# Performance work log

Measured on AMD Instinct MI355X. Metric: run time of the kernel, lower is better.

Reference implementation:

```python
import jax, jax.numpy as jnp
import numpy as np

N_TOKEN = 8192
N_EMBED = 512
DECAY = 0.99
EPS = 1e-08


def setup_inputs() -> dict:
    key = jax.random.key(0)
    k1, k2, k3, k4 = jax.random.split(key, 4)
    inputs = jax.random.normal(k1, (4, 4096, N_EMBED), dtype=jnp.float32)
    key_w = jax.random.normal(k2, (N_TOKEN, N_EMBED), dtype=jnp.float32)
    value_w = jax.random.normal(k3, (N_TOKEN, N_EMBED), dtype=jnp.float32)
    ema_n = jnp.ones((N_TOKEN,), dtype=jnp.float32)
    ema_w = jax.random.normal(k4, (N_TOKEN, N_EMBED), dtype=jnp.float32)
    return {"inputs": inputs, "key_w": key_w, "value_w": value_w,
            "ema_n": ema_n, "ema_w": ema_w}


def reference(inputs, key_w, value_w, ema_n, ema_w):
    size = inputs.shape
    x = inputs.reshape(-1, N_EMBED)  # [T, D]

    # squared euclidean distances to key codebook: [T, n_token]
    dists = (jnp.sum(x * x, axis=-1, keepdims=True)
             + jnp.sum(key_w * key_w, axis=-1)[None, :]
             - 2.0 * jnp.matmul(x, key_w.T))
    indices = jnp.argmin(dists, axis=-1)  # [T] int

    quantized = (x + value_w[indices]).reshape(size)

    # --- training-mode EMA codebook update (torch .data ops, no grad) ---
    T = x.shape[0]
    ratio = float(N_TOKEN) / T
    # cnts[k] = ratio * (#tokens assigned to k)
    cnts = jnp.zeros((N_TOKEN,), dtype=x.dtype).at[indices].add(ratio)
    # ws = one_hot(indices).T @ x scaled by ratio  (segment sum over codes)
    ws = jax.ops.segment_sum(x, indices, num_segments=N_TOKEN) * ratio
    ema_n_new = ema_n * DECAY + (1.0 - DECAY) * cnts
    ema_w_new = ema_w * DECAY + (1.0 - DECAY) * ws
    # renormalize keys (Laplace-smoothed counts)
    n = jnp.sum(ema_n_new)
    sz = (ema_n_new + EPS) / (n + EPS * N_TOKEN) * n
    key_w_new = ema_w_new / sz[:, None]

    return quantized, ema_n_new, ema_w_new, key_w_new
```

## Files before the change

kernel.cpp:

```cpp
#include <hip/hip_runtime.h>

#define N_TOKEN 8192
#define N_EMBED 512
#define T_TOKENS 16384
#define KP 1536
#define MARGIN 0.6f

typedef __bf16 bf16x8 __attribute__((ext_vector_type(8)));
typedef __bf16 bf16x4 __attribute__((ext_vector_type(4)));
typedef float f32x4 __attribute__((ext_vector_type(4)));

__device__ __forceinline__ unsigned int fkey(float f) {
  unsigned int u = __float_as_uint(f);
  return (u & 0x80000000u) ? ~u : (u | 0x80000000u);
}
__device__ __forceinline__ void gl2lds16(const void* gsrc, void* lds) {
  __builtin_amdgcn_global_load_lds(
      (const __attribute__((address_space(1))) unsigned int*)gsrc,
      (__attribute__((address_space(3))) unsigned int*)lds, 16, 0, 0);
}
__device__ __forceinline__ unsigned long long umin64(unsigned long long a,
                                                     unsigned long long b) {
  return a < b ? a : b;
}

__global__ void k_pack_x(const float* __restrict__ x, __bf16* __restrict__ xp) {
  int gid = blockIdx.x * blockDim.x + threadIdx.x;
  int t = gid >> 7, d4 = gid & 127;
  float4 v = reinterpret_cast<const float4*>(x)[gid];
  bf16x4 hi, lo;
  hi[0] = (__bf16)v.x; hi[1] = (__bf16)v.y; hi[2] = (__bf16)v.z; hi[3] = (__bf16)v.w;
  lo[0] = (__bf16)(v.x - (float)hi[0]);
  lo[1] = (__bf16)(v.y - (float)hi[1]);
  lo[2] = (__bf16)(v.z - (float)hi[2]);
  lo[3] = (__bf16)(v.w - (float)hi[3]);
  __bf16* row = xp + (size_t)t * KP + d4 * 4;
  *(bf16x4*)(row)        = hi;
  *(bf16x4*)(row + 512)  = hi;
  *(bf16x4*)(row + 1024) = lo;
}

__global__ void k_pack_k_norm(const float* __restrict__ kw, __bf16* __restrict__ kp,
                              float* __restrict__ h) {
  int row = blockIdx.x * 4 + (threadIdx.x >> 6);
  int lane = threadIdx.x & 63;
  const float4* src = reinterpret_cast<const float4*>(kw + (size_t)row * N_EMBED);
  __bf16* dst = kp + (size_t)row * KP;
  float s = 0.f;
  #pragma unroll
  for (int c = 0; c < 2; ++c) {
    int f4 = lane + c * 64;
    float4 v = src[f4];
    s += v.x*v.x + v.y*v.y + v.z*v.z + v.w*v.w;
    bf16x4 hi, lo;
    hi[0] = (__bf16)v.x; hi[1] = (__bf16)v.y; hi[2] = (__bf16)v.z; hi[3] = (__bf16)v.w;
    lo[0] = (__bf16)(v.x - (float)hi[0]);
    lo[1] = (__bf16)(v.y - (float)hi[1]);
    lo[2] = (__bf16)(v.z - (float)hi[2]);
    lo[3] = (__bf16)(v.w - (float)hi[3]);
    *(bf16x4*)(dst + f4 * 4)        = hi;
    *(bf16x4*)(dst + 512 + f4 * 4)  = lo;
    *(bf16x4*)(dst + 1024 + f4 * 4) = hi;
  }
  #pragma unroll
  for (int off = 32; off; off >>= 1) s += __shfl_down(s, off);
  if (lane == 0) h[row] = 0.5f * s;
}

__global__ void k_hnorm(const float* __restrict__ key_w, float* __restrict__ h) {
  int code = blockIdx.x * 4 + (threadIdx.x >> 6);
  int lane = threadIdx.x & 63;
  const float4* row = reinterpret_cast<const float4*>(key_w + (size_t)code * N_EMBED);
  float s = 0.f;
  float4 v0 = row[lane];
  float4 v1 = row[lane + 64];
  s += v0.x*v0.x + v0.y*v0.y + v0.z*v0.z + v0.w*v0.w;
  s += v1.x*v1.x + v1.y*v1.y + v1.z*v1.z + v1.w*v1.w;
  #pragma unroll
  for (int off = 32; off; off >>= 1) s += __shfl_down(s, off);
  if (lane == 0) h[code] = 0.5f * s;
}

#define BMr 128
#define BNr 128
#define BKe 64

__global__ __launch_bounds__(256) void k_mfma_top2(
    const __bf16* __restrict__ xp, const __bf16* __restrict__ kp,
    const float* __restrict__ h, float4* __restrict__ slots) {
  __shared__ __bf16 AS[BMr * BKe];
  __shared__ __bf16 BS[BNr * BKe];

  const int nb = blockIdx.x, mb = blockIdx.y;
  const int m0 = mb * BMr, n0 = nb * BNr;
  const int tid = threadIdx.x;
  const int lane = tid & 63;
  const int wid = tid >> 6;
  const int wm = wid * 32;

  f32x4 acc[2][8] = {};
  const int soff = tid * 16;

  for (int ks = 0; ks < 512; ks += BKe) {
    __syncthreads();
    #pragma unroll
    for (int i = 0; i < 4; ++i) {
      int off = i * 4096 + soff;
      int row = off >> 7;
      int inner = (off & 127) ^ ((row & 7) << 4);
      gl2lds16(xp + (size_t)(m0 + row) * KP + ks + (inner >> 1), (char*)AS + off);
      gl2lds16(kp + (size_t)(n0 + row) * KP + ks + (inner >> 1), (char*)BS + off);
    }
    asm volatile("s_waitcnt vmcnt(0)" ::: "memory");
    __syncthreads();

    #pragma unroll
    for (int kk = 0; kk < 2; ++kk) {
      const int cbyte = kk * 64 + (lane >> 4) * 16;
      bf16x8 af[2], bb[8];
      #pragma unroll
      for (int i = 0; i < 2; ++i) {
        int arow = wm + i * 16 + (lane & 15);
        af[i] = *(const bf16x8*)((const char*)AS + arow * 128 + (cbyte ^ ((arow & 7) << 4)));
      }
      #pragma unroll
      for (int j = 0; j < 8; ++j) {
        int brow = j * 16 + (lane & 15);
        bb[j] = *(const bf16x8*)((const char*)BS + brow * 128 + (cbyte ^ ((brow & 7) << 4)));
      }
      #pragma unroll
      for (int i = 0; i < 2; ++i)
        #pragma unroll
        for (int j = 0; j < 8; ++j)
          acc[i][j] = __builtin_amdgcn_mfma_f32_16x16x32_bf16(af[i], bb[j], acc[i][j], 0, 0, 0);
    }
  }

  const int rgrp = lane >> 4;
  const int cidx = lane & 15;
  #pragma unroll
  for (int i = 0; i < 2; ++i) {
    #pragma unroll
    for (int r = 0; r < 4; ++r) {
      float s1 = 3.4e38f, s2 = 3.4e38f;
      int c1 = 0;
      #pragma unroll
      for (int j = 0; j < 8; ++j) {
        int kk = n0 + j * 16 + cidx;
        float sc = h[kk] - acc[i][j][r];
        if (sc < s1) { s2 = s1; s1 = sc; c1 = kk; }
        else s2 = fminf(s2, sc);
      }
      #pragma unroll
      for (int msk = 1; msk < 16; msk <<= 1) {
        float o1 = __shfl_xor(s1, msk);
        float o2 = __shfl_xor(s2, msk);
        int   oc = __shfl_xor(c1, msk);
        float ns2 = fminf(fminf(s2, o2), fmaxf(s1, o1));
        bool take = o1 < s1;
        s1 = take ? o1 : s1;
        c1 = take ? oc : c1;
        s2 = ns2;
      }
      if (cidx == 0) {
        int row = m0 + wm + i * 16 + rgrp * 4 + r;
        float4 p;
        p.x = s1; p.y = s2; p.z = __int_as_float(c1); p.w = 0.f;
        slots[(size_t)row * 64 + nb] = p;
      }
    }
  }
}

__global__ void k_top2_reduce(const float4* __restrict__ slots,
                              int* __restrict__ idx, unsigned int* __restrict__ tlist,
                              unsigned int* __restrict__ ucount,
                              int* __restrict__ counts) {
  int row = blockIdx.x * 4 + (threadIdx.x >> 6);
  int lane = threadIdx.x & 63;
  float4 a = slots[(size_t)row * 64 + lane];
  float s1 = a.x, s2 = a.y; int c1 = __float_as_int(a.z);
  #pragma unroll
  for (int msk = 1; msk < 64; msk <<= 1) {
    float o1 = __shfl_xor(s1, msk);
    float o2 = __shfl_xor(s2, msk);
    int   oc = __shfl_xor(c1, msk);
    float ns2 = fminf(fminf(s2, o2), fmaxf(s1, o1));
    bool take = o1 < s1;
    s1 = take ? o1 : s1;
    c1 = take ? oc : c1;
    s2 = ns2;
  }
  if (lane == 0) {
    if (s2 - s1 >= MARGIN) {
      idx[row] = c1;
      atomicAdd(&counts[c1], 1);
    } else {
      unsigned int p = atomicAdd(ucount, 1u);
      tlist[p] = (unsigned int)row;
    }
  }
}

__global__ __launch_bounds__(256) void k_mfma_refine(
    const __bf16* __restrict__ xp, const __bf16* __restrict__ kp,
    const float* __restrict__ h, const unsigned int* __restrict__ tlist,
    const unsigned int* __restrict__ ucount, unsigned long long* __restrict__ rbest) {
  const unsigned int uc = *ucount;
  const int nb = blockIdx.x, mb = blockIdx.y;
  const int m0 = mb * BMr;
  if ((unsigned int)m0 >= uc) return;

  __shared__ __bf16 AS[BMr * BKe];
  __shared__ __bf16 BS[BNr * BKe];

  const int n0 = nb * BNr;
  const int tid = threadIdx.x;
  const int lane = tid & 63;
  const int wid = tid >> 6;
  const int wm = (wid >> 1) * 64, wn = (wid & 1) * 64;

  const int r0 = tid >> 3;
  size_t abase[4];
  #pragma unroll
  for (int i = 0; i < 4; ++i) {
    int p = m0 + r0 + 32 * i;
    int pc = p < (int)uc ? p : (int)uc - 1;
    abase[i] = (size_t)tlist[pc] * KP;
  }

  f32x4 acc[4][4] = {};
  const int soff = tid * 16;
  const int innerC = (soff & 127) ^ ((r0 & 7) << 4);

  for (int ks = 0; ks < KP; ks += BKe) {
    __syncthreads();
    #pragma unroll
    for (int i = 0; i < 4; ++i) {
      int off = i * 4096 + soff;
      int brow = (off >> 7);
      gl2lds16(xp + abase[i] + ks + (innerC >> 1), (char*)AS + off);
      int binner = (off & 127) ^ ((brow & 7) << 4);
      gl2lds16(kp + (size_t)(n0 + brow) * KP + ks + (binner >> 1), (char*)BS + off);
    }
    asm volatile("s_waitcnt vmcnt(0)" ::: "memory");
    __syncthreads();

    #pragma unroll
    for (int kk = 0; kk < 2; ++kk) {
      const int cbyte = kk * 64 + (lane >> 4) * 16;
      bf16x8 af[4], bb[4];
      #pragma unroll
      for (int i = 0; i < 4; ++i) {
        int arow = wm + i * 16 + (lane & 15);
        af[i] = *(const bf16x8*)((const char*)AS + arow * 128 + (cbyte ^ ((arow & 7) << 4)));
        int brow = wn + i * 16 + (lane & 15);
        bb[i] = *(const bf16x8*)((const char*)BS + brow * 128 + (cbyte ^ ((brow & 7) << 4)));
      }
      #pragma unroll
      for (int i = 0; i < 4; ++i)
        #pragma unroll
        for (int j = 0; j < 4; ++j)
          acc[i][j] = __builtin_amdgcn_mfma_f32_16x16x32_bf16(af[i], bb[j], acc[i][j], 0, 0, 0);
    }
  }

  const int rgrp = lane >> 4;
  const int cidx = lane & 15;
  #pragma unroll
  for (int i = 0; i < 4; ++i) {
    #pragma unroll
    for (int r = 0; r < 4; ++r) {
      unsigned long long m = ~0ull;
      #pragma unroll
      for (int j = 0; j < 4; ++j) {
        int kk = n0 + wn + j * 16 + cidx;
        float score = h[kk] - acc[i][j][r];
        unsigned long long cand =
            ((unsigned long long)fkey(score) << 32) | (unsigned int)kk;
        m = umin64(m, cand);
      }
      #pragma unroll
      for (int msk = 1; msk < 16; msk <<= 1) m = umin64(m, __shfl_xor(m, msk));
      if (cidx == 0) {
        int p = m0 + wm + i * 16 + rgrp * 4 + r;
        if ((unsigned int)p < uc) atomicMin(&rbest[p], m);
      }
    }
  }
}

__global__ void k_finalize(const unsigned long long* __restrict__ rbest,
                           const unsigned int* __restrict__ tlist,
                           const unsigned int* __restrict__ ucount,
                           int* __restrict__ idx, int* __restrict__ counts) {
  unsigned int p = blockIdx.x * 256 + threadIdx.x;
  if (p < *ucount) {
    int k = (int)(unsigned int)(rbest[p] & 0xffffffffull);
    idx[tlist[p]] = k;
    atomicAdd(&counts[k], 1);
  }
}

__global__ void k_sum_ema_n(const float* __restrict__ ema_n, float* __restrict__ nsum) {
  __shared__ float sm[256];
  float s = 0.f;
  for (int i = threadIdx.x; i < N_TOKEN; i += 256) s += ema_n[i];
  sm[threadIdx.x] = s;
  __syncthreads();
  for (int off = 128; off; off >>= 1) {
    if (threadIdx.x < off) sm[threadIdx.x] += sm[threadIdx.x + off];
    __syncthreads();
  }
  if (threadIdx.x == 0) *nsum = sm[0];
}

__global__ void k_scan(const int* __restrict__ counts, int* __restrict__ offs,
                       int* __restrict__ cursor) {
  __shared__ int sa[256], sb[256];
  int tid = threadIdx.x;
  int base = tid * 32;
  int loc[32]; int s = 0;
  #pragma unroll
  for (int e = 0; e < 32; ++e) { loc[e] = s; s += counts[base + e]; }
  sa[tid] = s;
  __syncthreads();
  int* src = sa; int* dst = sb;
  for (int d = 1; d < 256; d <<= 1) {
    int v = src[tid] + (tid >= d ? src[tid - d] : 0);
    dst[tid] = v;
    __syncthreads();
    int* tmp = src; src = dst; dst = tmp;
  }
  int excl = src[tid] - s;
  #pragma unroll
  for (int e = 0; e < 32; ++e) {
    int o = excl + loc[e];
    offs[base + e] = o;
    cursor[base + e] = o;
  }
}

__global__ void k_place(const int* __restrict__ idx, int* __restrict__ cursor,
                        int* __restrict__ tok) {
  int t = blockIdx.x * 256 + threadIdx.x;
  if (t < T_TOKENS) {
    int p = atomicAdd(&cursor[idx[t]], 1);
    tok[p] = t;
  }
}

__global__ void k_update(const float* __restrict__ x, const float* __restrict__ ema_n,
                         const float* __restrict__ ema_w, const int* __restrict__ counts,
                         const int* __restrict__ offs, const int* __restrict__ tok,
                         const float* __restrict__ nsum,
                         float* __restrict__ out_en, float* __restrict__ out_ew,
                         float* __restrict__ out_kw) {
  int k = blockIdx.x * 4 + (threadIdx.x >> 6);
  int lane = threadIdx.x & 63;
  int cnt = counts[k];
  int off = offs[k];
  float en = 0.99f * ema_n[k] + 0.005f * (float)cnt;
  if (lane == 0) out_en[k] = en;
  float n = 0.99f * (*nsum) + 81.92f;
  float sz = (en + 1e-8f) / (n + 1e-8f * (float)N_TOKEN) * n;

  const float4* er = reinterpret_cast<const float4*>(ema_w + (size_t)k * N_EMBED);
  float4 e0 = er[lane], e1 = er[lane + 64];
  float4 s0 = {0.f, 0.f, 0.f, 0.f}, s1v = {0.f, 0.f, 0.f, 0.f};
  for (int q = 0; q < cnt; ++q) {
    int t = tok[off + q];
    const float4* xr = reinterpret_cast<const float4*>(x + (size_t)t * N_EMBED);
    float4 a = xr[lane], b = xr[lane + 64];
    s0.x += a.x; s0.y += a.y; s0.z += a.z; s0.w += a.w;
    s1v.x += b.x; s1v.y += b.y; s1v.z += b.z; s1v.w += b.w;
  }
  float4 w0, w1;
  w0.x = 0.99f * e0.x + 0.005f * s0.x;  w0.y = 0.99f * e0.y + 0.005f * s0.y;
  w0.z = 0.99f * e0.z + 0.005f * s0.z;  w0.w = 0.99f * e0.w + 0.005f * s0.w;
  w1.x = 0.99f * e1.x + 0.005f * s1v.x; w1.y = 0.99f * e1.y + 0.005f * s1v.y;
  w1.z = 0.99f * e1.z + 0.005f * s1v.z; w1.w = 0.99f * e1.w + 0.005f * s1v.w;
  float4* ow = reinterpret_cast<float4*>(out_ew + (size_t)k * N_EMBED);
  ow[lane] = w0; ow[lane + 64] = w1;
  float4 q0, q1;
  q0.x = w0.x / sz; q0.y = w0.y / sz; q0.z = w0.z / sz; q0.w = w0.w / sz;
  q1.x = w1.x / sz; q1.y = w1.y / sz; q1.z = w1.z / sz; q1.w = w1.w / sz;
  float4* okw = reinterpret_cast<float4*>(out_kw + (size_t)k * N_EMBED);
  okw[lane] = q0; okw[lane + 64] = q1;
}

__global__ void k_quant(const float* __restrict__ x, const float* __restrict__ value_w,
                        const int* __restrict__ idx, float* __restrict__ q) {
  int gid = blockIdx.x * blockDim.x + threadIdx.x;
  int t = gid >> 7, d4 = gid & 127;
  float4 xv = reinterpret_cast<const float4*>(x)[gid];
  float4 v = reinterpret_cast<const float4*>(value_w + (size_t)idx[t] * N_EMBED)[d4];
  float4 o;
  o.x = xv.x + v.x; o.y = xv.y + v.y; o.z = xv.z + v.z; o.w = xv.w + v.w;
  reinterpret_cast<float4*>(q)[gid] = o;
}

__global__ __launch_bounds__(256) void k_mfma_argmin(
    const __bf16* __restrict__ xp, const __bf16* __restrict__ kp,
    const float* __restrict__ h, unsigned long long* __restrict__ best) {
  __shared__ __bf16 AS[BMr * BKe];
  __shared__ __bf16 BS[BNr * BKe];
  const int nb = blockIdx.x, mb = blockIdx.y;
  const int m0 = mb * BMr, n0 = nb * BNr;
  const int tid = threadIdx.x;
  const int lane = tid & 63;
  const int wid = tid >> 6;
  const int wm = (wid >> 1) * 64, wn = (wid & 1) * 64;
  f32x4 acc[4][4] = {};
  const int soff = tid * 16;
  for (int ks = 0; ks < KP; ks += BKe) {
    __syncthreads();
    #pragma unroll
    for (int i = 0; i < 4; ++i) {
      int off = i * 4096 + soff;
      int row = off >> 7;
      int inner = (off & 127) ^ ((row & 7) << 4);
      gl2lds16(xp + (size_t)(m0 + row) * KP + ks + (inner >> 1), (char*)AS + off);
      gl2lds16(kp + (size_t)(n0 + row) * KP + ks + (inner >> 1), (char*)BS + off);
    }
    asm volatile("s_waitcnt vmcnt(0)" ::: "memory");
    __syncthreads();
    #pragma unroll
    for (int kk = 0; kk < 2; ++kk) {
      const int cbyte = kk * 64 + (lane >> 4) * 16;
      bf16x8 af[4], bb[4];
      #pragma unroll
      for (int i = 0; i < 4; ++i) {
        int arow = wm + i * 16 + (lane & 15);
        af[i] = *(const bf16x8*)((const char*)AS + arow * 128 + (cbyte ^ ((arow & 7) << 4)));
        int brow = wn + i * 16 + (lane & 15);
        bb[i] = *(const bf16x8*)((const char*)BS + brow * 128 + (cbyte ^ ((brow & 7) << 4)));
      }
      #pragma unroll
      for (int i = 0; i < 4; ++i)
        #pragma unroll
        for (int j = 0; j < 4; ++j)
          acc[i][j] = __builtin_amdgcn_mfma_f32_16x16x32_bf16(af[i], bb[j], acc[i][j], 0, 0, 0);
    }
  }
  const int rgrp = lane >> 4;
  const int cidx = lane & 15;
  #pragma unroll
  for (int i = 0; i < 4; ++i) {
    #pragma unroll
    for (int r = 0; r < 4; ++r) {
      unsigned long long m = ~0ull;
      #pragma unroll
      for (int j = 0; j < 4; ++j) {
        int kk = n0 + wn + j * 16 + cidx;
        float score = h[kk] - acc[i][j][r];
        unsigned long long cand =
            ((unsigned long long)fkey(score) << 32) | (unsigned int)kk;
        m = umin64(m, cand);
      }
      #pragma unroll
      for (int msk = 1; msk < 16; msk <<= 1) m = umin64(m, __shfl_xor(m, msk));
      if (cidx == 0) {
        int row = m0 + wm + i * 16 + rgrp * 4 + r;
        atomicMin(&best[row], m);
      }
    }
  }
}

#define BT 128
#define BK 128
#define DC 32
__global__ __launch_bounds__(256, 2) void k_gemm_argmin(
    const float* __restrict__ x, const float* __restrict__ key_w,
    const float* __restrict__ h, unsigned long long* __restrict__ best) {
  __shared__ float4 XS[BT * 8];
  __shared__ float4 KS[BK * 8];
  const int kb = blockIdx.x, tb = blockIdx.y;
  const int t0 = tb * BT, k0 = kb * BK;
  const int tid = threadIdx.x;
  const int tx = tid & 15;
  const int tyg = tid >> 4;
  float acc[8][8];
  #pragma unroll
  for (int i = 0; i < 8; ++i)
    #pragma unroll
    for (int j = 0; j < 8; ++j) acc[i][j] = 0.f;
  for (int dc = 0; dc < N_EMBED; dc += DC) {
    __syncthreads();
    #pragma unroll
    for (int ld = 0; ld < 4; ++ld) {
      int li = ld * 256 + tid;
      int row = li >> 3, c4 = li & 7;
      XS[row * 8 + (c4 ^ (row & 7))] =
          *reinterpret_cast<const float4*>(x + (size_t)(t0 + row) * N_EMBED + dc + c4 * 4);
      KS[row * 8 + (c4 ^ (row & 7))] =
          *reinterpret_cast<const float4*>(key_w + (size_t)(k0 + row) * N_EMBED + dc + c4 * 4);
    }
    __syncthreads();
    #pragma unroll
    for (int d4 = 0; d4 < 8; ++d4) {
      float4 a[8], b[8];
      #pragma unroll
      for (int j = 0; j < 8; ++j) {
        a[j] = XS[(tyg + 16 * j) * 8 + (d4 ^ (tyg & 7))];
        b[j] = KS[(tx  + 16 * j) * 8 + (d4 ^ (tx  & 7))];
      }
      #pragma unroll
      for (int i = 0; i < 8; ++i) {
        float4 av = a[i];
        #pragma unroll
        for (int j = 0; j < 8; ++j) {
          float4 bv = b[j];
          acc[i][j] = fmaf(av.x, bv.x, fmaf(av.y, bv.y,
                      fmaf(av.z, bv.z, fmaf(av.w, bv.w, acc[i][j]))));
        }
      }
    }
  }
  #pragma unroll
  for (int i = 0; i < 8; ++i) {
    unsigned long long m = ~0ull;
    #pragma unroll
    for (int j = 0; j < 8; ++j) {
      int kk = k0 + tx + 16 * j;
      float score = h[kk] - acc[i][j];
      unsigned long long cand =
          ((unsigned long long)fkey(score) << 32) | (unsigned int)kk;
      m = umin64(m, cand);
    }
    #pragma unroll
    for (int mask = 1; mask < 16; mask <<= 1) m = umin64(m, __shfl_xor(m, mask));
    if (tx == 0) atomicMin(&best[t0 + tyg + 16 * i], m);
  }
}

__global__ void k_extract_counts(const unsigned long long* __restrict__ best,
                                 int* __restrict__ idx, float* __restrict__ out_en) {
  int t = blockIdx.x * blockDim.x + threadIdx.x;
  if (t < T_TOKENS) {
    int k = (int)(unsigned int)(best[t] & 0xffffffffull);
    idx[t] = k;
    atomicAdd(&out_en[k], 0.005f);
  }
}
__global__ void k_quant_scatter(const float* __restrict__ x,
                                const float* __restrict__ value_w,
                                const int* __restrict__ idx,
                                float* __restrict__ q, float* __restrict__ out_ew) {
  int gid = blockIdx.x * blockDim.x + threadIdx.x;
  int t = gid >> 7, d4 = gid & 127;
  float4 xv = reinterpret_cast<const float4*>(x)[gid];
  int k = idx[t];
  float4 v = reinterpret_cast<const float4*>(value_w + (size_t)k * N_EMBED)[d4];
  float4 o;
  o.x = xv.x + v.x; o.y = xv.y + v.y; o.z = xv.z + v.z; o.w = xv.w + v.w;
  reinterpret_cast<float4*>(q)[gid] = o;
  const float c = 0.005f;
  float* dst = out_ew + (size_t)k * N_EMBED + d4 * 4;
  atomicAdd(dst + 0, c * xv.x);
  atomicAdd(dst + 1, c * xv.y);
  atomicAdd(dst + 2, c * xv.z);
  atomicAdd(dst + 3, c * xv.w);
}
__global__ void k_scaleN(const float* __restrict__ ema_n, float* __restrict__ out_en) {
  int k = blockIdx.x * blockDim.x + threadIdx.x;
  if (k < N_TOKEN) out_en[k] = 0.99f * ema_n[k];
}
__global__ void k_scaleW(const float* __restrict__ ema_w, float* __restrict__ out_ew) {
  int gid = blockIdx.x * blockDim.x + threadIdx.x;
  float4 v = reinterpret_cast<const float4*>(ema_w)[gid];
  float4 o;
  o.x = 0.99f * v.x; o.y = 0.99f * v.y; o.z = 0.99f * v.z; o.w = 0.99f * v.w;
  reinterpret_cast<float4*>(out_ew)[gid] = o;
}
__global__ void k_sumn(const float* __restrict__ en, float* __restrict__ nsum) {
  __shared__ float sm[256];
  float s = 0.f;
  for (int i = threadIdx.x; i < N_TOKEN; i += 256) s += en[i];
  sm[threadIdx.x] = s;
  __syncthreads();
  for (int off = 128; off; off >>= 1) {
    if (threadIdx.x < off) sm[threadIdx.x] += sm[threadIdx.x + off];
    __syncthreads();
  }
  if (threadIdx.x == 0) *nsum = sm[0];
}
__global__ void k_keyw(const float* __restrict__ out_ew, const float* __restrict__ out_en,
                       const float* __restrict__ nsum, float* __restrict__ out_kw) {
  int gid = blockIdx.x * blockDim.x + threadIdx.x;
  int k = gid >> 7;
  float n = *nsum;
  float sz = (out_en[k] + 1e-8f) / (n + 1e-8f * (float)N_TOKEN) * n;
  float4 w = reinterpret_cast<const float4*>(out_ew)[gid];
  float4 o;
  o.x = w.x / sz; o.y = w.y / sz; o.z = w.z / sz; o.w = w.w / sz;
  reinterpret_cast<float4*>(out_kw)[gid] = o;
}

extern "C" void kernel_launch(void* const* d_in, const int* in_sizes, int n_in,
                              void* d_out, int out_size, void* d_ws, size_t ws_size,
                              hipStream_t stream) {
  const float* x       = (const float*)d_in[0];
  const float* key_w   = (const float*)d_in[1];
  const float* value_w = (const float*)d_in[2];
  const float* ema_n   = (const float*)d_in[3];
  const float* ema_w   = (const float*)d_in[4];

  float* out_q  = (float*)d_out;
  float* out_en = out_q + 8388608;
  float* out_ew = out_en + N_TOKEN;
  float* out_kw = out_ew + 4194304;

  const size_t SLOTS_B = (size_t)T_TOKENS * 64 * 16;
  const size_t XP_B    = (size_t)T_TOKENS * KP * 2;
  const size_t KP_B    = (size_t)N_TOKEN * KP * 2;
  char* base = (char*)d_ws;
  float4* slots = (float4*)base;
  __bf16* xp3 = (__bf16*)(base + SLOTS_B);
  __bf16* kp3 = (__bf16*)(base + SLOTS_B + XP_B);
  char* tail  = base + SLOTS_B + XP_B + KP_B;
  float* h                  = (float*)(tail + 0);
  int*   idx                = (int*)(tail + 32768);
  unsigned int* tlist       = (unsigned int*)(tail + 98304);
  unsigned long long* rbest = (unsigned long long*)(tail + 163840);
  unsigned int* ucount      = (unsigned int*)(tail + 294912);
  float* nsum               = (float*)(tail + 295168);
  int* counts               = (int*)(tail + 295424);
  int* offs                 = (int*)(tail + 328192);
  int* cursor               = (int*)(tail + 360960);
  int* tok                  = (int*)(tail + 393728);
  const size_t ws_need2 = SLOTS_B + XP_B + KP_B + 459264;

  unsigned long long* f_best = (unsigned long long*)d_ws;
  int*   f_idx  = (int*)((char*)d_ws + 131072);
  float* f_h    = (float*)((char*)d_ws + 196608);
  float* f_nsum = (float*)((char*)d_ws + 229376);
  __bf16* f_xp  = (__bf16*)((char*)d_ws + 262144);
  __bf16* f_kp  = (__bf16*)((char*)d_ws + 262144 + XP_B);
  const size_t ws_need1 = 262144 + XP_B + KP_B;

  if (ws_size >= ws_need2) {
    hipMemsetAsync(rbest, 0xFF, (size_t)T_TOKENS * 8, stream);
    hipMemsetAsync(ucount, 0, 4, stream);
    hipMemsetAsync(counts, 0, N_TOKEN * 4, stream);
    k_sum_ema_n<<<1, 256, 0, stream>>>(ema_n, nsum);
    k_pack_x<<<(T_TOKENS * (N_EMBED / 4)) / 256, 256, 0, stream>>>(x, xp3);
    k_pack_k_norm<<<N_TOKEN / 4, 256, 0, stream>>>(key_w, kp3, h);
    {
      dim3 grid(N_TOKEN / BNr, T_TOKENS / BMr);
      k_mfma_top2<<<grid, 256, 0, stream>>>(xp3, kp3, h, slots);
    }
    k_top2_reduce<<<T_TOKENS / 4, 256, 0, stream>>>(slots, idx, tlist, ucount, counts);
    {
      dim3 grid(N_TOKEN / BNr, T_TOKENS / BMr);
      k_mfma_refine<<<grid, 256, 0, stream>>>(xp3, kp3, h, tlist, ucount, rbest);
    }
    k_finalize<<<T_TOKENS / 256, 256, 0, stream>>>(rbest, tlist, ucount, idx, counts);

    k_scan<<<1, 256, 0, stream>>>(counts, offs, cursor);
    k_place<<<T_TOKENS / 256, 256, 0, stream>>>(idx, cursor, tok);
    k_update<<<N_TOKEN / 4, 256, 0, stream>>>(x, ema_n, ema_w, counts, offs, tok,
                                              nsum, out_en, out_ew, out_kw);
    k_quant<<<(T_TOKENS * (N_EMBED / 4)) / 256, 256, 0, stream>>>(x, value_w, idx, out_q);
  } else if (ws_size >= ws_need1) {
    hipMemsetAsync(f_best, 0xFF, (size_t)T_TOKENS * 8, stream);
    k_pack_x<<<(T_TOKENS * (N_EMBED / 4)) / 256, 256, 0, stream>>>(x, f_xp);
    k_pack_k_norm<<<N_TOKEN / 4, 256, 0, stream>>>(key_w, f_kp, f_h);
    dim3 grid(N_TOKEN / BNr, T_TOKENS / BMr);
    k_mfma_argmin<<<grid, 256, 0, stream>>>(f_xp, f_kp, f_h, f_best);

    k_scaleN<<<N_TOKEN / 256, 256, 0, stream>>>(ema_n, out_en);
    k_extract_counts<<<T_TOKENS / 256, 256, 0, stream>>>(f_best, f_idx, out_en);
    k_scaleW<<<(N_TOKEN * (N_EMBED / 4)) / 256, 256, 0, stream>>>(ema_w, out_ew);
    k_quant_scatter<<<(T_TOKENS * (N_EMBED / 4)) / 256, 256, 0, stream>>>(
        x, value_w, f_idx, out_q, out_ew);
    k_sumn<<<1, 256, 0, stream>>>(out_en, f_nsum);
    k_keyw<<<(N_TOKEN * (N_EMBED / 4)) / 256, 256, 0, stream>>>(out_ew, out_en, f_nsum, out_kw);
  } else {
    hipMemsetAsync(f_best, 0xFF, (size_t)T_TOKENS * 8, stream);
    k_hnorm<<<N_TOKEN / 4, 256, 0, stream>>>(key_w, f_h);
    dim3 grid(N_TOKEN / BK, T_TOKENS / BT);
    k_gemm_argmin<<<grid, 256, 0, stream>>>(x, key_w, f_h, f_best);

    k_scaleN<<<N_TOKEN / 256, 256, 0, stream>>>(ema_n, out_en);
    k_extract_counts<<<T_TOKENS / 256, 256, 0, stream>>>(f_best, f_idx, out_en);
    k_scaleW<<<(N_TOKEN * (N_EMBED / 4)) / 256, 256, 0, stream>>>(ema_w, out_ew);
    k_quant_scatter<<<(T_TOKENS * (N_EMBED / 4)) / 256, 256, 0, stream>>>(
        x, value_w, f_idx, out_q, out_ew);
    k_sumn<<<1, 256, 0, stream>>>(out_en, f_nsum);
    k_keyw<<<(N_TOKEN * (N_EMBED / 4)) / 256, 256, 0, stream>>>(out_ew, out_en, f_nsum, out_kw);
  }
}
```

Measured before the change: 442.0 us.

## Sweep four code tiles per block in top2, fuse quant into update

```diff
diff --git a/kernel.cpp b/kernel.cpp
--- a/kernel.cpp
+++ b/kernel.cpp
@@ -91,83 +91,99 @@
   __shared__ __bf16 AS[BMr * BKe];
   __shared__ __bf16 BS[BNr * BKe];
 
-  const int nb = blockIdx.x, mb = blockIdx.y;
-  const int m0 = mb * BMr, n0 = nb * BNr;
+  const int nbg = blockIdx.x, mb = blockIdx.y;
+  const int m0 = mb * BMr;
   const int tid = threadIdx.x;
   const int lane = tid & 63;
   const int wid = tid >> 6;
   const int wm = wid * 32;
-
-  f32x4 acc[2][8] = {};
   const int soff = tid * 16;
-
-  for (int ks = 0; ks < 512; ks += BKe) {
-    __syncthreads();
-    #pragma unroll
-    for (int i = 0; i < 4; ++i) {
-      int off = i * 4096 + soff;
-      int row = off >> 7;
-      int inner = (off & 127) ^ ((row & 7) << 4);
-      gl2lds16(xp + (size_t)(m0 + row) * KP + ks + (inner >> 1), (char*)AS + off);
-      gl2lds16(kp + (size_t)(n0 + row) * KP + ks + (inner >> 1), (char*)BS + off);
-    }
-    asm volatile("s_waitcnt vmcnt(0)" ::: "memory");
-    __syncthreads();
-
-    #pragma unroll
-    for (int kk = 0; kk < 2; ++kk) {
-      const int cbyte = kk * 64 + (lane >> 4) * 16;
-      bf16x8 af[2], bb[8];
-      #pragma unroll
-      for (int i = 0; i < 2; ++i) {
-        int arow = wm + i * 16 + (lane & 15);
-        af[i] = *(const bf16x8*)((const char*)AS + arow * 128 + (cbyte ^ ((arow & 7) << 4)));
-      }
-      #pragma unroll
-      for (int j = 0; j < 8; ++j) {
-        int brow = j * 16 + (lane & 15);
-        bb[j] = *(const bf16x8*)((const char*)BS + brow * 128 + (cbyte ^ ((brow & 7) << 4)));
-      }
-      #pragma unroll
-      for (int i = 0; i < 2; ++i)
-        #pragma unroll
-        for (int j = 0; j < 8; ++j)
-          acc[i][j] = __builtin_amdgcn_mfma_f32_16x16x32_bf16(af[i], bb[j], acc[i][j], 0, 0, 0);
-    }
-  }
-
   const int rgrp = lane >> 4;
   const int cidx = lane & 15;
-  #pragma unroll
-  for (int i = 0; i < 2; ++i) {
-    #pragma unroll
-    for (int r = 0; r < 4; ++r) {
-      float s1 = 3.4e38f, s2 = 3.4e38f;
-      int c1 = 0;
-      #pragma unroll
-      for (int j = 0; j < 8; ++j) {
-        int kk = n0 + j * 16 + cidx;
-        float sc = h[kk] - acc[i][j][r];
-        if (sc < s1) { s2 = s1; s1 = sc; c1 = kk; }
-        else s2 = fminf(s2, sc);
-      }
-      #pragma unroll
-      for (int msk = 1; msk < 16; msk <<= 1) {
-        float o1 = __shfl_xor(s1, msk);
-        float o2 = __shfl_xor(s2, msk);
-        int   oc = __shfl_xor(c1, msk);
-        float ns2 = fminf(fminf(s2, o2), fmaxf(s1, o1));
-        bool take = o1 < s1;
-        s1 = take ? o1 : s1;
-        c1 = take ? oc : c1;
-        s2 = ns2;
-      }
-      if (cidx == 0) {
-        int row = m0 + wm + i * 16 + rgrp * 4 + r;
-        float4 p;
-        p.x = s1; p.y = s2; p.z = __int_as_float(c1); p.w = 0.f;
-        slots[(size_t)row * 64 + nb] = p;
-      }
+
+  float rs1[8], rs2[8];
+  int rc1[8];
+  #pragma unroll
+  for (int u = 0; u < 8; ++u) { rs1[u] = 3.4e38f; rs2[u] = 3.4e38f; rc1[u] = 0; }
+
+  for (int q = 0; q < 4; ++q) {
+    const int n0 = (nbg * 4 + q) * BNr;
+    f32x4 acc[2][8] = {};
+
+    for (int ks = 0; ks < 512; ks += BKe) {
+      __syncthreads();
+      #pragma unroll
+      for (int i = 0; i < 4; ++i) {
+        int off = i * 4096 + soff;
+        int row = off >> 7;
+        int inner = (off & 127) ^ ((row & 7) << 4);
+        gl2lds16(xp + (size_t)(m0 + row) * KP + ks + (inner >> 1), (char*)AS + off);
+        gl2lds16(kp + (size_t)(n0 + row) * KP + ks + (inner >> 1), (char*)BS + off);
+      }
+      asm volatile("s_waitcnt vmcnt(0)" ::: "memory");
+      __syncthreads();
+
+      #pragma unroll
+      for (int kk = 0; kk < 2; ++kk) {
+        const int cbyte = kk * 64 + (lane >> 4) * 16;
+        bf16x8 af[2], bb[8];
+        #pragma unroll
+        for (int i = 0; i < 2; ++i) {
+          int arow = wm + i * 16 + (lane & 15);
+          af[i] = *(const bf16x8*)((const char*)AS + arow * 128 + (cbyte ^ ((arow & 7) << 4)));
+        }
+        #pragma unroll
+        for (int j = 0; j < 8; ++j) {
+          int brow = j * 16 + (lane & 15);
+          bb[j] = *(const bf16x8*)((const char*)BS + brow * 128 + (cbyte ^ ((brow & 7) << 4)));
+        }
+        #pragma unroll
+        for (int i = 0; i < 2; ++i)
+          #pragma unroll
+          for (int j = 0; j < 8; ++j)
+            acc[i][j] = __builtin_amdgcn_mfma_f32_16x16x32_bf16(af[i], bb[j], acc[i][j], 0, 0, 0);
+      }
+    }
+
+    #pragma unroll
+    for (int i = 0; i < 2; ++i) {
+      #pragma unroll
+      for (int r = 0; r < 4; ++r) {
+        const int u = i * 4 + r;
+        float s1 = rs1[u], s2 = rs2[u];
+        int c1 = rc1[u];
+        #pragma unroll
+        for (int j = 0; j < 8; ++j) {
+          int kk = n0 + j * 16 + cidx;
+          float sc = h[kk] - acc[i][j][r];
+          if (sc < s1) { s2 = s1; s1 = sc; c1 = kk; }
+          else s2 = fminf(s2, sc);
+        }
+        rs1[u] = s1; rs2[u] = s2; rc1[u] = c1;
+      }
+    }
+  }
+
+  #pragma unroll
+  for (int u = 0; u < 8; ++u) {
+    float s1 = rs1[u], s2 = rs2[u];
+    int c1 = rc1[u];
+    #pragma unroll
+    for (int msk = 1; msk < 16; msk <<= 1) {
+      float o1 = __shfl_xor(s1, msk);
+      float o2 = __shfl_xor(s2, msk);
+      int   oc = __shfl_xor(c1, msk);
+      float ns2 = fminf(fminf(s2, o2), fmaxf(s1, o1));
+      bool take = o1 < s1;
+      s1 = take ? o1 : s1;
+      c1 = take ? oc : c1;
+      s2 = ns2;
+    }
+    if (cidx == 0) {
+      int row = m0 + wm + (u >> 2) * 16 + rgrp * 4 + (u & 3);
+      float4 p;
+      p.x = s1; p.y = s2; p.z = __int_as_float(c1); p.w = 0.f;
+      slots[(size_t)row * 16 + nbg] = p;
     }
   }
 }
@@ -175,13 +191,17 @@
 __global__ void k_top2_reduce(const float4* __restrict__ slots,
                               int* __restrict__ idx, unsigned int* __restrict__ tlist,
                               unsigned int* __restrict__ ucount,
-                              int* __restrict__ counts) {
-  int row = blockIdx.x * 4 + (threadIdx.x >> 6);
-  int lane = threadIdx.x & 63;
-  float4 a = slots[(size_t)row * 64 + lane];
-  float s1 = a.x, s2 = a.y; int c1 = __float_as_int(a.z);
-  #pragma unroll
-  for (int msk = 1; msk < 64; msk <<= 1) {
+                              int* __restrict__ counts,
+                              unsigned long long* __restrict__ rbest) {
+  int tid = threadIdx.x;
+  int lane = tid & 63, wid = tid >> 6;
+  int row = blockIdx.x * 16 + wid * 4 + (lane >> 4);
+  int slot = lane & 15;
+  float4 a = slots[(size_t)row * 16 + slot];
+  float s1 = a.x, s2 = a.y;
+  int c1 = __float_as_int(a.z);
+  #pragma unroll
+  for (int msk = 1; msk < 16; msk <<= 1) {
     float o1 = __shfl_xor(s1, msk);
     float o2 = __shfl_xor(s2, msk);
     int   oc = __shfl_xor(c1, msk);
@@ -191,13 +211,14 @@
     c1 = take ? oc : c1;
     s2 = ns2;
   }
-  if (lane == 0) {
+  if (slot == 0) {
     if (s2 - s1 >= MARGIN) {
       idx[row] = c1;
       atomicAdd(&counts[c1], 1);
     } else {
       unsigned int p = atomicAdd(ucount, 1u);
       tlist[p] = (unsigned int)row;
+      rbest[p] = ~0ull;
     }
   }
 }
@@ -351,11 +372,12 @@
 }
 
 __global__ void k_update(const float* __restrict__ x, const float* __restrict__ ema_n,
-                         const float* __restrict__ ema_w, const int* __restrict__ counts,
+                         const float* __restrict__ ema_w, const float* __restrict__ value_w,
+                         const int* __restrict__ counts,
                          const int* __restrict__ offs, const int* __restrict__ tok,
                          const float* __restrict__ nsum,
                          float* __restrict__ out_en, float* __restrict__ out_ew,
-                         float* __restrict__ out_kw) {
+                         float* __restrict__ out_kw, float* __restrict__ out_q) {
   int k = blockIdx.x * 4 + (threadIdx.x >> 6);
   int lane = threadIdx.x & 63;
   int cnt = counts[k];
@@ -367,6 +389,8 @@
 
   const float4* er = reinterpret_cast<const float4*>(ema_w + (size_t)k * N_EMBED);
   float4 e0 = er[lane], e1 = er[lane + 64];
+  const float4* vr = reinterpret_cast<const float4*>(value_w + (size_t)k * N_EMBED);
+  float4 v0 = vr[lane], v1 = vr[lane + 64];
   float4 s0 = {0.f, 0.f, 0.f, 0.f}, s1v = {0.f, 0.f, 0.f, 0.f};
   for (int q = 0; q < cnt; ++q) {
     int t = tok[off + q];
@@ -374,6 +398,11 @@
     float4 a = xr[lane], b = xr[lane + 64];
     s0.x += a.x; s0.y += a.y; s0.z += a.z; s0.w += a.w;
     s1v.x += b.x; s1v.y += b.y; s1v.z += b.z; s1v.w += b.w;
+    float4 qa, qb;
+    qa.x = a.x + v0.x; qa.y = a.y + v0.y; qa.z = a.z + v0.z; qa.w = a.w + v0.w;
+    qb.x = b.x + v1.x; qb.y = b.y + v1.y; qb.z = b.z + v1.z; qb.w = b.w + v1.w;
+    float4* oq = reinterpret_cast<float4*>(out_q + (size_t)t * N_EMBED);
+    oq[lane] = qa; oq[lane + 64] = qb;
   }
   float4 w0, w1;
   w0.x = 0.99f * e0.x + 0.005f * s0.x;  w0.y = 0.99f * e0.y + 0.005f * s0.y;
@@ -612,7 +641,7 @@
   float* out_ew = out_en + N_TOKEN;
   float* out_kw = out_ew + 4194304;
 
-  const size_t SLOTS_B = (size_t)T_TOKENS * 64 * 16;
+  const size_t SLOTS_B = (size_t)T_TOKENS * 16 * 16;
   const size_t XP_B    = (size_t)T_TOKENS * KP * 2;
   const size_t KP_B    = (size_t)N_TOKEN * KP * 2;
   char* base = (char*)d_ws;
@@ -641,17 +670,17 @@
   const size_t ws_need1 = 262144 + XP_B + KP_B;
 
   if (ws_size >= ws_need2) {
-    hipMemsetAsync(rbest, 0xFF, (size_t)T_TOKENS * 8, stream);
     hipMemsetAsync(ucount, 0, 4, stream);
     hipMemsetAsync(counts, 0, N_TOKEN * 4, stream);
     k_sum_ema_n<<<1, 256, 0, stream>>>(ema_n, nsum);
     k_pack_x<<<(T_TOKENS * (N_EMBED / 4)) / 256, 256, 0, stream>>>(x, xp3);
     k_pack_k_norm<<<N_TOKEN / 4, 256, 0, stream>>>(key_w, kp3, h);
     {
-      dim3 grid(N_TOKEN / BNr, T_TOKENS / BMr);
+      dim3 grid(N_TOKEN / (BNr * 4), T_TOKENS / BMr);
       k_mfma_top2<<<grid, 256, 0, stream>>>(xp3, kp3, h, slots);
     }
-    k_top2_reduce<<<T_TOKENS / 4, 256, 0, stream>>>(slots, idx, tlist, ucount, counts);
+    k_top2_reduce<<<T_TOKENS / 16, 256, 0, stream>>>(slots, idx, tlist, ucount,
+                                                     counts, rbest);
     {
       dim3 grid(N_TOKEN / BNr, T_TOKENS / BMr);
       k_mfma_refine<<<grid, 256, 0, stream>>>(xp3, kp3, h, tlist, ucount, rbest);
@@ -660,9 +689,9 @@
 
     k_scan<<<1, 256, 0, stream>>>(counts, offs, cursor);
     k_place<<<T_TOKENS / 256, 256, 0, stream>>>(idx, cursor, tok);
-    k_update<<<N_TOKEN / 4, 256, 0, stream>>>(x, ema_n, ema_w, counts, offs, tok,
-                                              nsum, out_en, out_ew, out_kw);
-    k_quant<<<(T_TOKENS * (N_EMBED / 4)) / 256, 256, 0, stream>>>(x, value_w, idx, out_q);
+    k_update<<<N_TOKEN / 4, 256, 0, stream>>>(x, ema_n, ema_w, value_w, counts,
+                                              offs, tok, nsum,
+                                              out_en, out_ew, out_kw, out_q);
   } else if (ws_size >= ws_need1) {
     hipMemsetAsync(f_best, 0xFF, (size_t)T_TOKENS * 8, stream);
     k_pack_x<<<(T_TOKENS * (N_EMBED / 4)) / 256, 256, 0, stream>>>(x, f_xp);
```

Result: faster. 415.4 us (-6.0%).
